# Kernel optimization log

Hardware: AMD Instinct MI355X
Metric: run time of the kernel (lower is better)

Reference implementation:

```python
import jax, jax.numpy as jnp
import numpy as np

B, S, D, H = 4, 1024, 1024, 16
HD = D // H  # head_dim = 64
MASKED_BIAS = -10000.0


def setup_inputs() -> dict:
    key = jax.random.key(0)
    ks = jax.random.split(key, 7)
    sc = 0.02
    return {
        "hidden_states": jax.random.normal(ks[0], (B, S, D), jnp.float32),
        "textual_key": jax.random.normal(ks[1], (B, H, S, HD), jnp.float32),
        "textual_value": jax.random.normal(ks[2], (B, H, S, HD), jnp.float32),
        "Wc": jax.random.normal(ks[3], (D, 3 * D), jnp.float32) * sc,  # Conv1D c_attn
        "bc": jnp.zeros((3 * D,), jnp.float32),
        "Wp": jax.random.normal(ks[4], (D, D), jnp.float32) * sc,  # Conv1D c_proj
        "bp": jnp.zeros((D,), jnp.float32),
    }


def reference(hidden_states, textual_key, textual_value, Wc, bc, Wp, bp):
    b, s, d = hidden_states.shape
    # Conv1D: x @ W + b, then split into q, k, v
    qkv = hidden_states @ Wc + bc  # [B,S,3D]
    q, k, v = jnp.split(qkv, 3, axis=-1)

    def split_heads(t):  # [B,S,D] -> [B,H,S,HD]
        return t.reshape(b, s, H, HD).transpose(0, 2, 1, 3)

    q, k, v = split_heads(q), split_heads(k), split_heads(v)

    # cross-key scores against textual past + fused elementwise self-term
    text_w = jnp.einsum("bhqd,bhkd->bhqk", q, textual_key)  # [B,H,S,S_kv]
    self_w = jnp.sum(q * k, axis=-1, keepdims=True)  # [B,H,S,1]
    attn_w = jnp.concatenate([text_w, self_w], axis=-1) / (HD ** 0.5)

    # nonResidual causal mask: bias[kl-ql:kl, 1:kl+1] (strict lower-tri since
    # columns are shifted by 1) concatenated with an always-true self column
    i = jnp.arange(s)
    causal = i[None, :] < i[:, None]  # [S,S_kv]: allow k < q (strict)
    mask = jnp.concatenate([causal, jnp.ones((s, 1), bool)], axis=-1)[None, None]
    attn_w = jnp.where(mask, attn_w, jnp.asarray(MASKED_BIAS, attn_w.dtype))
    attn_w = jax.nn.softmax(attn_w, axis=-1)

    w_rest, w_self = attn_w[..., :-1], attn_w[..., -1:]
    out = jnp.einsum("bhqk,bhkd->bhqd", w_rest, textual_value) + w_self * v

    out = out.transpose(0, 2, 1, 3).reshape(b, s, d)  # merge heads
    return out @ Wp + bp
```

## Files before the change

### kernel.cpp

```cpp
#include <hip/hip_runtime.h>

typedef __bf16 bf16_t;
typedef __bf16 bf16x8 __attribute__((ext_vector_type(8)));
typedef __bf16 bf16x4 __attribute__((ext_vector_type(4)));
typedef _Float16 f16x4 __attribute__((ext_vector_type(4)));
typedef float f32x4 __attribute__((ext_vector_type(4)));

__device__ __forceinline__ void gl_lds16(const void* g, void* l) {
  __builtin_amdgcn_global_load_lds(
      (const __attribute__((address_space(1))) unsigned int*)g,
      (__attribute__((address_space(3))) unsigned int*)l, 16, 0, 0);
}

__global__ __launch_bounds__(256) void prep_kernel(
    const float* __restrict__ hs, const float* __restrict__ tk, const float* __restrict__ tv,
    const float* __restrict__ Wc, const float* __restrict__ Wp,
    bf16_t* __restrict__ Ahs, bf16_t* __restrict__ Ktb, _Float16* __restrict__ Vtb,
    bf16_t* __restrict__ WcT, bf16_t* __restrict__ WpT) {
  const int blk = blockIdx.x;
  if (blk < 8192) {
    const float4* src = (blk < 4096) ? (const float4*)hs : (const float4*)tk;
    bf16x4* dst = (blk < 4096) ? (bf16x4*)Ahs : (bf16x4*)Ktb;
    int i = (blk & 4095) * 256 + threadIdx.x;
    float4 v = src[i];
    bf16x4 o;
    o[0] = (bf16_t)v.x; o[1] = (bf16_t)v.y; o[2] = (bf16_t)v.z; o[3] = (bf16_t)v.w;
    dst[i] = o;
  } else {
    __shared__ float tile[32][33];
    const int x = threadIdx.x & 31, y0 = threadIdx.x >> 5;
    const float* in; bf16_t* out; int C, c0, r0; size_t base; bool isV = false;
    if (blk < 11264) {
      int t = blk - 8192; in = Wc; out = WcT; C = 3072; base = 0;
      c0 = (t % 96) * 32; r0 = (t / 96) * 32;
    } else if (blk < 12288) {
      int t = blk - 11264; in = Wp; out = WpT; C = 1024; base = 0;
      c0 = (t & 31) * 32; r0 = (t >> 5) * 32;
    } else {
      int t = blk - 12288; int z = t >> 6, rest = t & 63;
      in = tv; out = nullptr; isV = true; C = 64; base = (size_t)z * 65536;
      c0 = (rest & 1) * 32; r0 = (rest >> 1) * 32;
    }
#pragma unroll
    for (int k = 0; k < 4; k++) {
      int y = y0 + 8 * k;
      tile[y][x] = in[base + (size_t)(r0 + y) * C + c0 + x];
    }
    __syncthreads();
#pragma unroll
    for (int k = 0; k < 4; k++) {
      int y = y0 + 8 * k;
      if (isV)
        Vtb[base + (size_t)(c0 + y) * 1024 + r0 + x] = (_Float16)tile[x][y];
      else
        out[base + (size_t)(c0 + y) * 1024 + r0 + x] = (bf16_t)tile[x][y];
    }
  }
}

#define ATTN_M 12.0f
__global__ __launch_bounds__(512, 4) void fused_attn_kernel(
    const bf16_t* __restrict__ Ahs, const bf16_t* __restrict__ WcT,
    const float* __restrict__ bc,
    const bf16_t* __restrict__ Ktxt, const _Float16* __restrict__ VtxtT,
    bf16_t* __restrict__ Aout) {
  const int bh = blockIdx.x;
  const int qt = blockIdx.y;
  const int b = bh >> 4, h = bh & 15;
  const int tid = threadIdx.x, wave = tid >> 6, lane = tid & 63;
  const int c = lane & 15, qd = lane >> 4;
  const int i_base = qt * 128 + wave * 16;
  const int kt_max = 2 * qt + 1;
  const int m0 = b * 1024 + qt * 128;

  const bf16_t* Ktb = Ktxt + (size_t)bh * 65536;
  const _Float16* Vtb = VtxtT + (size_t)bh * 65536;

  __shared__ __align__(16) char pool[49152];
  bf16_t* Asm = (bf16_t*)pool;
  bf16_t* Bsm = (bf16_t*)(pool + 16384);
  bf16_t* Qsm = (bf16_t*)pool;
  bf16_t* KsmB = (bf16_t*)(pool + 16384);
  _Float16* VsmB = (_Float16*)(pool + 32768);

  f32x4 acc[12];
#pragma unroll
  for (int j = 0; j < 12; j++) acc[j] = (f32x4){0.f, 0.f, 0.f, 0.f};

  for (int kt = 0; kt < 16; kt++) {
#pragma unroll
    for (int p = 0; p < 2; p++) {
      int chunk = p * 512 + tid;
      int row = chunk >> 3, sb = chunk & 7, kb = sb ^ (row & 7);
      gl_lds16(Ahs + (size_t)(m0 + row) * 1024 + kt * 64 + kb * 8, Asm + chunk * 8);
    }
#pragma unroll
    for (int p = 0; p < 3; p++) {
      int chunk = p * 512 + tid;
      int brow = chunk >> 3, sb = chunk & 7, kb = sb ^ (brow & 7);
      int wrow = (brow >> 6) * 1024 + h * 64 + (brow & 63);
      gl_lds16(WcT + (size_t)wrow * 1024 + kt * 64 + kb * 8, Bsm + chunk * 8);
    }
    __syncthreads();
#pragma unroll
    for (int kk = 0; kk < 2; kk++) {
      int arow = wave * 16 + c;
      bf16x8 af = *(const bf16x8*)(&Asm[arow * 64 + (((4 * kk + qd) ^ (arow & 7)) << 3)]);
#pragma unroll
      for (int j = 0; j < 12; j++) {
        int brow = 16 * j + c;
        bf16x8 bf = *(const bf16x8*)(&Bsm[brow * 64 + (((4 * kk + qd) ^ (brow & 7)) << 3)]);
        acc[j] = __builtin_amdgcn_mfma_f32_16x16x32_bf16(af, bf, acc[j], 0, 0, 0);
      }
    }
    __syncthreads();
  }

  {
    int row = tid >> 3, sb = tid & 7, kb = sb ^ (row & 7);
    gl_lds16(Ktb + (size_t)row * 64 + kb * 8, KsmB + tid * 8);
    gl_lds16(Vtb + (size_t)row * 1024 + kb * 8, VsmB + tid * 8);
  }

#pragma unroll
  for (int j = 0; j < 12; j++) {
    float bv = bc[(j >> 2) * 1024 + h * 64 + 16 * (j & 3) + c];
#pragma unroll
    for (int r = 0; r < 4; r++) acc[j][r] += bv;
  }

  float wself[4];
#pragma unroll
  for (int r = 0; r < 4; r++) {
    float part = acc[0][r] * acc[4][r] + acc[1][r] * acc[5][r] +
                 acc[2][r] * acc[6][r] + acc[3][r] * acc[7][r];
#pragma unroll
    for (int mk = 1; mk < 16; mk <<= 1) part += __shfl_xor(part, mk, 64);
    wself[r] = __expf(part * 0.125f - ATTN_M);
  }

  f32x4 O[4];
#pragma unroll
  for (int u = 0; u < 4; u++)
#pragma unroll
    for (int r = 0; r < 4; r++) O[u][r] = wself[r] * acc[8 + u][r];

  bf16_t* Qw = Qsm + wave * 1024;
#pragma unroll
  for (int j = 0; j < 4; j++) {
#pragma unroll
    for (int r = 0; r < 4; r++) {
      int ql = 4 * qd + r, d = 16 * j + c;
      int ch = (d >> 3) ^ (ql & 7);
      Qw[ql * 64 + (ch << 3) + (d & 7)] = (bf16_t)acc[j][r];
    }
  }
  bf16x8 aq[2];
#pragma unroll
  for (int kk = 0; kk < 2; kk++) {
    int ch = (4 * kk + qd) ^ (c & 7);
    aq[kk] = *(const bf16x8*)(&Qw[c * 64 + (ch << 3)]);
  }

  float l_loc = 0.f;
  for (int kt = 0; kt <= kt_max; kt++) {
    __syncthreads();
    if (kt < kt_max) {
      int nb = (kt + 1) & 1;
      int row = tid >> 3, sb = tid & 7, kb = sb ^ (row & 7);
      gl_lds16(Ktb + (size_t)((kt + 1) * 64 + row) * 64 + kb * 8, KsmB + nb * 4096 + tid * 8);
      gl_lds16(Vtb + (size_t)row * 1024 + (kt + 1) * 64 + kb * 8, VsmB + nb * 4096 + tid * 8);
    }
    if (64 * kt >= i_base + 16) continue;
    const bf16_t* Ks = KsmB + (kt & 1) * 4096;
    const _Float16* Vs = VsmB + (kt & 1) * 4096;

    f32x4 sc[4];
#pragma unroll
    for (int t = 0; t < 4; t++) sc[t] = (f32x4){0.f, 0.f, 0.f, 0.f};
#pragma unroll
    for (int kk = 0; kk < 2; kk++) {
#pragma unroll
      for (int t = 0; t < 4; t++) {
        int row = 16 * t + c;
        bf16x8 bk = *(const bf16x8*)(&Ks[row * 64 + (((4 * kk + qd) ^ (row & 7)) << 3)]);
        sc[t] = __builtin_amdgcn_mfma_f32_16x16x32_bf16(bk, aq[kk], sc[t], 0, 0, 0);
      }
    }
    const bool edge = (64 * kt + 63 >= i_base);
    f16x4 pa[4];
    if (!edge) {
#pragma unroll
      for (int t = 0; t < 4; t++)
#pragma unroll
        for (int r = 0; r < 4; r++) {
          float p = __expf(sc[t][r] * 0.125f - ATTN_M);
          l_loc += p;
          pa[t][r] = (_Float16)p;
        }
    } else {
#pragma unroll
      for (int t = 0; t < 4; t++)
#pragma unroll
        for (int r = 0; r < 4; r++) {
          bool masked = (64 * kt + 16 * t + 4 * qd + r >= i_base + c);
          float p = masked ? 0.f : __expf(sc[t][r] * 0.125f - ATTN_M);
          l_loc += p;
          pa[t][r] = (_Float16)p;
        }
    }
#pragma unroll
    for (int u = 0; u < 4; u++) {
      int row = 16 * u + c;
#pragma unroll
      for (int t = 0; t < 4; t++) {
        int kc = 2 * t + (qd >> 1);
        f16x4 vb = *(const f16x4*)(&Vs[row * 64 + ((kc ^ (row & 7)) << 3) + ((qd & 1) << 2)]);
        O[u] = __builtin_amdgcn_mfma_f32_16x16x16f16(pa[t], vb, O[u], 0, 0, 0);
      }
    }
  }

  l_loc += __shfl_xor(l_loc, 16, 64);
  l_loc += __shfl_xor(l_loc, 32, 64);
#pragma unroll
  for (int r = 0; r < 4; r++) {
    float lq = __shfl(l_loc, 4 * qd + r, 16);
    float inv = 1.0f / (lq + wself[r]);
    int i = i_base + 4 * qd + r;
#pragma unroll
    for (int u = 0; u < 4; u++)
      Aout[((size_t)b * 1024 + i) * 1024 + h * 64 + 16 * u + c] = (bf16_t)(O[u][r] * inv);
  }
}

__global__ __launch_bounds__(256) void gemm_out_kernel(
    const bf16_t* __restrict__ A, const bf16_t* __restrict__ Bt, const float* __restrict__ bias,
    float* __restrict__ out) {
  __shared__ bf16_t Asm[2][4096];
  __shared__ bf16_t Bsm[2][8192];
  const int tid = threadIdx.x;
  const int wave = tid >> 6, lane = tid & 63;
  const int c = lane & 15, qd = lane >> 4;
  const int wn = wave * 32;
  const int m0 = blockIdx.y * 64, n0 = blockIdx.x * 128;

  f32x4 acc[4][2];
#pragma unroll
  for (int i = 0; i < 4; i++)
#pragma unroll
    for (int j = 0; j < 2; j++) acc[i][j] = (f32x4){0.f, 0.f, 0.f, 0.f};

#pragma unroll
  for (int p = 0; p < 2; p++) {
    int chunk = p * 256 + tid;
    int row = chunk >> 3, sb = chunk & 7, kb = sb ^ (row & 7);
    gl_lds16(A + (size_t)(m0 + row) * 1024 + kb * 8, &Asm[0][chunk * 8]);
  }
#pragma unroll
  for (int p = 0; p < 4; p++) {
    int chunk = p * 256 + tid;
    int row = chunk >> 3, sb = chunk & 7, kb = sb ^ (row & 7);
    gl_lds16(Bt + (size_t)(n0 + row) * 1024 + kb * 8, &Bsm[0][chunk * 8]);
  }
  for (int it = 0; it < 16; it++) {
    __syncthreads();
    if (it < 15) {
      int nbuf = (it + 1) & 1, kt = (it + 1) * 64;
#pragma unroll
      for (int p = 0; p < 2; p++) {
        int chunk = p * 256 + tid;
        int row = chunk >> 3, sb = chunk & 7, kb = sb ^ (row & 7);
        gl_lds16(A + (size_t)(m0 + row) * 1024 + kt + kb * 8, &Asm[nbuf][chunk * 8]);
      }
#pragma unroll
      for (int p = 0; p < 4; p++) {
        int chunk = p * 256 + tid;
        int row = chunk >> 3, sb = chunk & 7, kb = sb ^ (row & 7);
        gl_lds16(Bt + (size_t)(n0 + row) * 1024 + kt + kb * 8, &Bsm[nbuf][chunk * 8]);
      }
    }
    const int bs = it & 1;
#pragma unroll
    for (int kk = 0; kk < 2; kk++) {
      bf16x8 af[4], bfr[2];
#pragma unroll
      for (int i = 0; i < 4; i++) {
        int row = 16 * i + c;
        af[i] = *(const bf16x8*)(&Asm[bs][row * 64 + (((4 * kk + qd) ^ (row & 7)) << 3)]);
      }
#pragma unroll
      for (int j = 0; j < 2; j++) {
        int row = wn + 16 * j + c;
        bfr[j] = *(const bf16x8*)(&Bsm[bs][row * 64 + (((4 * kk + qd) ^ (row & 7)) << 3)]);
      }
#pragma unroll
      for (int i = 0; i < 4; i++)
#pragma unroll
        for (int j = 0; j < 2; j++)
          acc[i][j] = __builtin_amdgcn_mfma_f32_16x16x32_bf16(af[i], bfr[j], acc[i][j], 0, 0, 0);
    }
  }
#pragma unroll
  for (int j = 0; j < 2; j++) {
    int n = n0 + wn + 16 * j + c;
    float bv = bias[n];
#pragma unroll
    for (int i = 0; i < 4; i++) {
#pragma unroll
      for (int r = 0; r < 4; r++) {
        int m = m0 + 16 * i + 4 * qd + r;
        out[(size_t)m * 1024 + n] = acc[i][j][r] + bv;
      }
    }
  }
}

extern "C" void kernel_launch(void* const* d_in, const int* in_sizes, int n_in,
                              void* d_out, int out_size, void* d_ws, size_t ws_size,
                              hipStream_t stream) {
  const float* hs = (const float*)d_in[0];
  const float* tk = (const float*)d_in[1];
  const float* tv = (const float*)d_in[2];
  const float* Wc = (const float*)d_in[3];
  const float* bc = (const float*)d_in[4];
  const float* Wp = (const float*)d_in[5];
  const float* bp = (const float*)d_in[6];
  float* out = (float*)d_out;

  bf16_t* ws = (bf16_t*)d_ws;
  const size_t M1 = 1u << 20;
  bf16_t* Ahs  = ws;
  bf16_t* WcT  = ws + 4 * M1;
  bf16_t* WpT  = ws + 7 * M1;
  bf16_t* Ktb  = ws + 8 * M1;
  _Float16* Vtb = (_Float16*)(ws + 12 * M1);
  bf16_t* Aout = ws + 28 * M1;

  prep_kernel<<<16384, 256, 0, stream>>>(hs, tk, tv, Wc, Wp, Ahs, Ktb, Vtb, WcT, WpT);
  fused_attn_kernel<<<dim3(64, 8), 512, 0, stream>>>(Ahs, WcT, bc, Ktb, Vtb, Aout);
  gemm_out_kernel<<<dim3(8, 64), 256, 0, stream>>>(Aout, WpT, bp, out);
}
```

Baseline: 177.3 us.

## Widen prep conversions, reorder causal q-tiles, and use wide V loads in attention

The prep kernel now has each thread convert 8 elements with wider vector loads and stores. Transposes use 64x32 tiles with 16-byte writes and a permuted column order for V, which halves the block count. The attention kernel remaps blockIdx.y so heavy and light causal q-tiles interleave for better load balance. The PV loop also loads 8 f16 V values at once and splits them across two MFMAs, which relies on the permuted V layout matching the new indexing.

Result: no change. 174.7 us (-1.5%).

```diff
diff --git a/kernel.cpp b/kernel.cpp
--- a/kernel.cpp
+++ b/kernel.cpp
@@ -4,6 +4,7 @@
 typedef __bf16 bf16x8 __attribute__((ext_vector_type(8)));
 typedef __bf16 bf16x4 __attribute__((ext_vector_type(4)));
 typedef _Float16 f16x4 __attribute__((ext_vector_type(4)));
+typedef _Float16 f16x8 __attribute__((ext_vector_type(8)));
 typedef float f32x4 __attribute__((ext_vector_type(4)));
 
 __device__ __forceinline__ void gl_lds16(const void* g, void* l) {
@@ -18,42 +19,55 @@
     bf16_t* __restrict__ Ahs, bf16_t* __restrict__ Ktb, _Float16* __restrict__ Vtb,
     bf16_t* __restrict__ WcT, bf16_t* __restrict__ WpT) {
   const int blk = blockIdx.x;
-  if (blk < 8192) {
-    const float4* src = (blk < 4096) ? (const float4*)hs : (const float4*)tk;
-    bf16x4* dst = (blk < 4096) ? (bf16x4*)Ahs : (bf16x4*)Ktb;
-    int i = (blk & 4095) * 256 + threadIdx.x;
-    float4 v = src[i];
-    bf16x4 o;
-    o[0] = (bf16_t)v.x; o[1] = (bf16_t)v.y; o[2] = (bf16_t)v.z; o[3] = (bf16_t)v.w;
+  const int tid = threadIdx.x;
+  if (blk < 4096) {
+    const float4* src = (blk < 2048) ? (const float4*)hs : (const float4*)tk;
+    bf16x8* dst = (blk < 2048) ? (bf16x8*)Ahs : (bf16x8*)Ktb;
+    int i = (blk & 2047) * 256 + tid;
+    float4 v0 = src[2 * i], v1 = src[2 * i + 1];
+    bf16x8 o;
+    o[0] = (bf16_t)v0.x; o[1] = (bf16_t)v0.y; o[2] = (bf16_t)v0.z; o[3] = (bf16_t)v0.w;
+    o[4] = (bf16_t)v1.x; o[5] = (bf16_t)v1.y; o[6] = (bf16_t)v1.z; o[7] = (bf16_t)v1.w;
     dst[i] = o;
   } else {
-    __shared__ float tile[32][33];
-    const int x = threadIdx.x & 31, y0 = threadIdx.x >> 5;
-    const float* in; bf16_t* out; int C, c0, r0; size_t base; bool isV = false;
-    if (blk < 11264) {
-      int t = blk - 8192; in = Wc; out = WcT; C = 3072; base = 0;
-      c0 = (t % 96) * 32; r0 = (t / 96) * 32;
-    } else if (blk < 12288) {
-      int t = blk - 11264; in = Wp; out = WpT; C = 1024; base = 0;
-      c0 = (t & 31) * 32; r0 = (t >> 5) * 32;
+    __shared__ float tile[32][65];
+    const float* in; bf16_t* out; int C, r0, c0; size_t base = 0; bool isV = false;
+    if (blk < 5632) {
+      int t = blk - 4096; in = Wc; out = WcT; C = 3072;
+      r0 = (t / 96) * 64; c0 = (t % 96) * 32;
+    } else if (blk < 6144) {
+      int t = blk - 5632; in = Wp; out = WpT; C = 1024;
+      r0 = (t >> 5) * 64; c0 = (t & 31) * 32;
     } else {
-      int t = blk - 12288; int z = t >> 6, rest = t & 63;
+      int t = blk - 6144; int z = t >> 5, rest = t & 31;
       in = tv; out = nullptr; isV = true; C = 64; base = (size_t)z * 65536;
-      c0 = (rest & 1) * 32; r0 = (rest >> 1) * 32;
-    }
-#pragma unroll
-    for (int k = 0; k < 4; k++) {
-      int y = y0 + 8 * k;
-      tile[y][x] = in[base + (size_t)(r0 + y) * C + c0 + x];
-    }
-    __syncthreads();
-#pragma unroll
-    for (int k = 0; k < 4; k++) {
-      int y = y0 + 8 * k;
-      if (isV)
-        Vtb[base + (size_t)(c0 + y) * 1024 + r0 + x] = (_Float16)tile[x][y];
-      else
-        out[base + (size_t)(c0 + y) * 1024 + r0 + x] = (bf16_t)tile[x][y];
+      r0 = (rest >> 1) * 64; c0 = (rest & 1) * 32;
+    }
+    {
+      int rr = tid >> 2, cq = (tid & 3) << 3;
+      const float* sp = in + base + (size_t)(r0 + rr) * C + c0 + cq;
+      float4 v0 = *(const float4*)sp, v1 = *(const float4*)(sp + 4);
+      tile[cq + 0][rr] = v0.x; tile[cq + 1][rr] = v0.y;
+      tile[cq + 2][rr] = v0.z; tile[cq + 3][rr] = v0.w;
+      tile[cq + 4][rr] = v1.x; tile[cq + 5][rr] = v1.y;
+      tile[cq + 6][rr] = v1.z; tile[cq + 7][rr] = v1.w;
+    }
+    __syncthreads();
+    int y = tid >> 3, l = tid & 7;
+    if (isV) {
+      f16x8 o;
+#pragma unroll
+      for (int j = 0; j < 8; j++) {
+        int k = ((l & 4) << 3) | ((j & 4) << 2) | ((l & 2) << 2) | ((l & 1) << 2) | (j & 3);
+        o[j] = (_Float16)tile[y][k];
+      }
+      *(f16x8*)(Vtb + base + (size_t)(c0 + y) * 1024 + r0 + (l << 3)) = o;
+    } else {
+      const float* rowp = &tile[y][l << 3];
+      bf16x8 o;
+#pragma unroll
+      for (int j = 0; j < 8; j++) o[j] = (bf16_t)rowp[j];
+      *(bf16x8*)(out + (size_t)(c0 + y) * 1024 + r0 + (l << 3)) = o;
     }
   }
 }
@@ -65,7 +79,8 @@
     const bf16_t* __restrict__ Ktxt, const _Float16* __restrict__ VtxtT,
     bf16_t* __restrict__ Aout) {
   const int bh = blockIdx.x;
-  const int qt = blockIdx.y;
+  const int y = blockIdx.y;
+  const int qt = (y < 4) ? y : 11 - y;
   const int b = bh >> 4, h = bh & 15;
   const int tid = threadIdx.x, wave = tid >> 6, lane = tid & 63;
   const int c = lane & 15, qd = lane >> 4;
@@ -210,13 +225,15 @@
         }
     }
 #pragma unroll
-    for (int u = 0; u < 4; u++) {
-      int row = 16 * u + c;
-#pragma unroll
-      for (int t = 0; t < 4; t++) {
-        int kc = 2 * t + (qd >> 1);
-        f16x4 vb = *(const f16x4*)(&Vs[row * 64 + ((kc ^ (row & 7)) << 3) + ((qd & 1) << 2)]);
-        O[u] = __builtin_amdgcn_mfma_f32_16x16x16f16(pa[t], vb, O[u], 0, 0, 0);
+    for (int tp = 0; tp < 2; tp++) {
+#pragma unroll
+      for (int u = 0; u < 4; u++) {
+        int row = 16 * u + c;
+        f16x8 vv = *(const f16x8*)(&Vs[row * 64 + (((4 * tp + qd) ^ (row & 7)) << 3)]);
+        f16x4 vlo = __builtin_shufflevector(vv, vv, 0, 1, 2, 3);
+        f16x4 vhi = __builtin_shufflevector(vv, vv, 4, 5, 6, 7);
+        O[u] = __builtin_amdgcn_mfma_f32_16x16x16f16(pa[2 * tp], vlo, O[u], 0, 0, 0);
+        O[u] = __builtin_amdgcn_mfma_f32_16x16x16f16(pa[2 * tp + 1], vhi, O[u], 0, 0, 0);
       }
     }
   }
@@ -337,7 +354,7 @@
   _Float16* Vtb = (_Float16*)(ws + 12 * M1);
   bf16_t* Aout = ws + 28 * M1;
 
-  prep_kernel<<<16384, 256, 0, stream>>>(hs, tk, tv, Wc, Wp, Ahs, Ktb, Vtb, WcT, WpT);
+  prep_kernel<<<8192, 256, 0, stream>>>(hs, tk, tv, Wc, Wp, Ahs, Ktb, Vtb, WcT, WpT);
   fused_attn_kernel<<<dim3(64, 8), 512, 0, stream>>>(Ahs, WcT, bc, Ktb, Vtb, Aout);
   gemm_out_kernel<<<dim3(8, 64), 256, 0, stream>>>(Aout, WpT, bp, out);
 }
```
